# Kernel optimization log

Measured on AMD Instinct MI355X. Metric: run time of the kernel, lower is better.

## Reference

```python
import jax, jax.numpy as jnp
import numpy as np
from jax import lax

L, B, T, C, F = 4, 4, 2048, 1024, 4096  # n_layer, batch, ctx_len, n_embd(=dim_att), dim_ffn
EPS = 1e-5


def setup_inputs() -> dict:
    key = jax.random.key(0)
    ks = jax.random.split(key, 16)
    s = 0.02
    d = {}
    d["x"] = jax.random.normal(ks[0], (B, T, C), jnp.float32)
    d["ln0_w"] = jnp.ones((C,), jnp.float32)
    d["ln0_b"] = jnp.zeros((C,), jnp.float32)
    d["ln1_w"] = jnp.ones((L, C), jnp.float32)
    d["ln1_b"] = jnp.zeros((L, C), jnp.float32)
    d["ln2_w"] = jnp.ones((L, C), jnp.float32)
    d["ln2_b"] = jnp.zeros((L, C), jnp.float32)
    d["time_decay"] = jax.random.normal(ks[1], (L, C), jnp.float32) * 0.5
    d["time_first"] = jax.random.normal(ks[2], (L, C), jnp.float32) * 0.5 + jnp.float32(np.log(0.3))
    d["tmk"] = jax.random.uniform(ks[3], (L, C), jnp.float32)
    d["tmv"] = jax.random.uniform(ks[4], (L, C), jnp.float32)
    d["tmr"] = jax.random.uniform(ks[5], (L, C), jnp.float32)
    d["Wk"] = jax.random.normal(ks[6], (L, C, C), jnp.float32) * s
    d["Wv"] = jax.random.normal(ks[7], (L, C, C), jnp.float32) * s
    d["Wr"] = jax.random.normal(ks[8], (L, C, C), jnp.float32) * s
    d["Wo"] = jax.random.normal(ks[9], (L, C, C), jnp.float32) * s
    d["cmk"] = jax.random.uniform(ks[10], (L, C), jnp.float32)
    d["cmr"] = jax.random.uniform(ks[11], (L, C), jnp.float32)
    d["Wck"] = jax.random.normal(ks[12], (L, F, C), jnp.float32) * s  # key: n_embd -> dim_ffn
    d["Wcv"] = jax.random.normal(ks[13], (L, C, F), jnp.float32) * s  # value: dim_ffn -> n_embd
    d["Wcr"] = jax.random.normal(ks[14], (L, C, C), jnp.float32) * s  # receptance
    return d


def layernorm(x, w, b):
    m = jnp.mean(x, axis=-1, keepdims=True)
    v = jnp.var(x, axis=-1, keepdims=True)
    return (x - m) * lax.rsqrt(v + EPS) * w + b


def time_shift(x):
    # ZeroPad2d((0,0,1,-1)): shift sequence right by one, zero at t=0
    return jnp.pad(x, ((0, 0), (1, 0), (0, 0)))[:, :-1]


def wkv(time_decay, time_first, k, v):
    # numerically-stable RWKV-4 WKV recurrence; k,v: [B,T,C]
    w = -jnp.exp(time_decay)  # [C]
    u = time_first            # [C]
    kt = jnp.swapaxes(k, 0, 1)  # [T,B,C]
    vt = jnp.swapaxes(v, 0, 1)
    Bn, Cn = k.shape[0], k.shape[2]
    init = (jnp.zeros((Bn, Cn), k.dtype), jnp.zeros((Bn, Cn), k.dtype),
            jnp.full((Bn, Cn), -1e38, k.dtype))

    def step(carry, kv):
        aa, bb, pp = carry
        kk, vv = kv
        ww = u + kk
        qq = jnp.maximum(pp, ww)
        e1 = jnp.exp(pp - qq)
        e2 = jnp.exp(ww - qq)
        out = (e1 * aa + e2 * vv) / (e1 * bb + e2)
        ww2 = pp + w
        qq2 = jnp.maximum(ww2, kk)
        e1b = jnp.exp(ww2 - qq2)
        e2b = jnp.exp(kk - qq2)
        return (e1b * aa + e2b * vv, e1b * bb + e2b, qq2), out

    _, out = lax.scan(step, init, (kt, vt))
    return jnp.swapaxes(out, 0, 1)  # [B,T,C]


def reference(x, ln0_w, ln0_b, ln1_w, ln1_b, ln2_w, ln2_b, time_decay, time_first,
              tmk, tmv, tmr, Wk, Wv, Wr, Wo, cmk, cmr, Wck, Wcv, Wcr):
    x = layernorm(x, ln0_w, ln0_b)  # ln0 on layer 0
    for l in range(L):
        # --- TimeMix ---
        h = layernorm(x, ln1_w[l], ln1_b[l])
        hh = time_shift(h)
        xk = h * tmk[l] + hh * (1 - tmk[l])
        xv = h * tmv[l] + hh * (1 - tmv[l])
        xr = h * tmr[l] + hh * (1 - tmr[l])
        k = jnp.einsum('btc,oc->bto', xk, Wk[l])
        v = jnp.einsum('btc,oc->bto', xv, Wv[l])
        sr = jax.nn.sigmoid(jnp.einsum('btc,oc->bto', xr, Wr[l]))
        rwkv = sr * wkv(time_decay[l], time_first[l], k, v)
        x = x + jnp.einsum('bto,co->btc', rwkv, Wo[l])
        # --- ChannelMix ---
        h = layernorm(x, ln2_w[l], ln2_b[l])
        hh = time_shift(h)
        xk = h * cmk[l] + hh * (1 - cmk[l])
        xr = h * cmr[l] + hh * (1 - cmr[l])
        kf = jnp.einsum('btc,fc->btf', xk, Wck[l])
        kf = jnp.square(jax.nn.relu(kf))
        kv = jnp.einsum('btf,cf->btc', kf, Wcv[l])
        x = x + jax.nn.sigmoid(jnp.einsum('btc,oc->bto', xr, Wcr[l])) * kv
    return x
```

## Files before the change

kernel.cpp:

```cpp
#include <hip/hip_runtime.h>
#include <cstdint>

#define TT 2048
#define CCH 1024
#define FFD 4096
#define EPSV 1e-5f
#define NCHK 32
#define CHKL 64

typedef __attribute__((ext_vector_type(4))) float floatx4;
typedef __attribute__((ext_vector_type(8))) short shortx8;

__device__ __forceinline__ unsigned short f32_to_bf16(float f){
  union { float f; unsigned int u; } x; x.f = f;
  unsigned int r = x.u + 0x7fffu + ((x.u >> 16) & 1u);
  return (unsigned short)(r >> 16);
}
__device__ __forceinline__ float bf16_to_f32(unsigned short h){
  union { unsigned int u; float f; } x; x.u = ((unsigned int)h) << 16;
  return x.f;
}
__device__ __forceinline__ float wave_sum(float v){
  #pragma unroll
  for (int o = 32; o > 0; o >>= 1) v += __shfl_down(v, o, 64);
  return v;
}
__device__ __forceinline__ void async16(const void* g, void* l){
  __builtin_amdgcn_global_load_lds((const __attribute__((address_space(1))) void*)g,
                                   (__attribute__((address_space(3))) void*)l, 16, 0, 0);
}

struct CvtArgs {
  const float* s[7];
  unsigned short* d[7];
  int n4[7];
};
__global__ __launch_bounds__(256) void cvt7_kernel(CvtArgs a){
  const int seg = blockIdx.y;
  const float* __restrict__ s = a.s[seg];
  unsigned short* __restrict__ d = a.d[seg];
  const int n4 = a.n4[seg];
  for (int i = blockIdx.x * 256 + threadIdx.x; i < n4; i += gridDim.x * 256) {
    float4 v = ((const float4*)s)[i];
    union { unsigned short u[4]; uint2 p; } o;
    o.u[0] = f32_to_bf16(v.x); o.u[1] = f32_to_bf16(v.y);
    o.u[2] = f32_to_bf16(v.z); o.u[3] = f32_to_bf16(v.w);
    *(uint2*)&d[(long)i * 4] = o.p;
  }
}

__global__ __launch_bounds__(256) void ln0_kernel(const float* __restrict__ xin,
    const float* __restrict__ w, const float* __restrict__ b, float* __restrict__ xo){
  const int row = blockIdx.x, tid = threadIdx.x;
  const float* xr = xin + (long)row * CCH;
  float c4[4]; float s = 0.f, s2 = 0.f;
  #pragma unroll
  for (int j = 0; j < 4; j++){ c4[j] = xr[tid + j*256]; s += c4[j]; s2 += c4[j]*c4[j]; }
  s = wave_sum(s); s2 = wave_sum(s2);
  __shared__ float red[2][4];
  const int wid = tid >> 6, lane = tid & 63;
  if (lane == 0){ red[0][wid] = s; red[1][wid] = s2; }
  __syncthreads();
  const float S  = red[0][0]+red[0][1]+red[0][2]+red[0][3];
  const float S2 = red[1][0]+red[1][1]+red[1][2]+red[1][3];
  const float inv = 1.f / CCH;
  const float m = S * inv;
  const float rs = rsqrtf(S2 * inv - m*m + EPSV);
  float* xout = xo + (long)row * CCH;
  #pragma unroll
  for (int j = 0; j < 4; j++){ int c = tid + j*256; xout[c] = (c4[j]-m)*rs*w[c] + b[c]; }
}

template<int NOUT>
__global__ __launch_bounds__(256) void ln_mix(
    const float* __restrict__ x,
    const float* __restrict__ lw, const float* __restrict__ lb,
    const float* __restrict__ mk, const float* __restrict__ mv, const float* __restrict__ mr,
    unsigned short* __restrict__ xk, unsigned short* __restrict__ xv, unsigned short* __restrict__ xr)
{
  const int row = blockIdx.x;
  const int t = row & (TT - 1);
  const int tid = threadIdx.x;
  const float* xc = x + (long)row * CCH;
  const float* xp = xc - CCH;
  float c4[4], p4[4];
  float s1=0.f, s2=0.f, s3=0.f, s4=0.f;
  #pragma unroll
  for (int j = 0; j < 4; j++){
    const int c = tid + j*256;
    c4[j] = xc[c];
    p4[j] = (t > 0) ? xp[c] : 0.f;
    s1 += c4[j]; s2 += c4[j]*c4[j];
    s3 += p4[j]; s4 += p4[j]*p4[j];
  }
  s1 = wave_sum(s1); s2 = wave_sum(s2); s3 = wave_sum(s3); s4 = wave_sum(s4);
  __shared__ float red[4][4];
  const int wid = tid >> 6, lane = tid & 63;
  if (lane == 0){ red[wid][0]=s1; red[wid][1]=s2; red[wid][2]=s3; red[wid][3]=s4; }
  __syncthreads();
  const float S1 = red[0][0]+red[1][0]+red[2][0]+red[3][0];
  const float S2 = red[0][1]+red[1][1]+red[2][1]+red[3][1];
  const float S3 = red[0][2]+red[1][2]+red[2][2]+red[3][2];
  const float S4 = red[0][3]+red[1][3]+red[2][3]+red[3][3];
  const float inv = 1.f / CCH;
  const float m1 = S1*inv; const float r1 = rsqrtf(S2*inv - m1*m1 + EPSV);
  const float m0 = S3*inv; const float r0 = rsqrtf(S4*inv - m0*m0 + EPSV);
  #pragma unroll
  for (int j = 0; j < 4; j++){
    const int c = tid + j*256;
    const long o = (long)row * CCH + c;
    const float wv = lw[c], bv = lb[c];
    const float h  = (c4[j]-m1)*r1*wv + bv;
    const float hp = (t > 0) ? ((p4[j]-m0)*r0*wv + bv) : 0.f;
    const float a = mk[c]; xk[o] = f32_to_bf16(h*a + hp*(1.f-a));
    if (NOUT == 3){ const float q = mv[c]; xv[o] = f32_to_bf16(h*q + hp*(1.f-q)); }
    const float g = mr[c]; xr[o] = f32_to_bf16(h*g + hp*(1.f-g));
  }
}

__global__ __launch_bounds__(256) void wkv_pass1(
    const unsigned short* __restrict__ kin, const unsigned short* __restrict__ vin,
    const float* __restrict__ td,
    float* __restrict__ sta, float* __restrict__ stb, float* __restrict__ stp)
{
  const int c = blockIdx.x * 256 + threadIdx.x;
  const int chunk = blockIdx.y, b = blockIdx.z;
  const float w = -__expf(td[c]);
  const long base = ((long)b * TT + (long)chunk * CHKL) * CCH + c;
  float aa = 0.f, bb = 0.f, pp = -1e38f;
  for (int t0 = 0; t0 < CHKL; t0 += 8) {
    float kr[8], vr[8];
    #pragma unroll
    for (int j = 0; j < 8; j++){
      const long o = base + (long)(t0 + j) * CCH;
      kr[j] = bf16_to_f32(kin[o]);
      vr[j] = bf16_to_f32(vin[o]);
    }
    #pragma unroll
    for (int j = 0; j < 8; j++){
      const float kk = kr[j], vv = vr[j];
      const float ww2 = pp + w;
      const float qq2 = fmaxf(ww2, kk);
      const float e1b = __expf(ww2 - qq2), e2b = __expf(kk - qq2);
      aa = e1b*aa + e2b*vv; bb = e1b*bb + e2b; pp = qq2;
    }
  }
  const long si = (long)chunk * 4096 + b * CCH + c;
  sta[si] = aa; stb[si] = bb; stp[si] = pp;
}

__global__ __launch_bounds__(256) void wkv_combine(
    const float* __restrict__ td,
    const float* __restrict__ sta, const float* __restrict__ stb, const float* __restrict__ stp,
    float* __restrict__ ina, float* __restrict__ inb, float* __restrict__ inp)
{
  const int idx = blockIdx.x * 256 + threadIdx.x;
  const int c = idx & (CCH - 1);
  const float wn = -__expf(td[c]) * (float)CHKL;
  float a = 0.f, b = 0.f, p = -1e38f;
  for (int j0 = 0; j0 < NCHK; j0 += 8) {
    float la[8], lb[8], lp[8];
    #pragma unroll
    for (int j = 0; j < 8; j++){
      const long si = (long)(j0 + j) * 4096 + idx;
      la[j] = sta[si]; lb[j] = stb[si]; lp[j] = stp[si];
    }
    #pragma unroll
    for (int j = 0; j < 8; j++){
      const long si = (long)(j0 + j) * 4096 + idx;
      ina[si] = a; inb[si] = b; inp[si] = p;
      const float pd = p + wn;
      const float q = fmaxf(pd, lp[j]);
      const float e1 = __expf(pd - q), e2 = __expf(lp[j] - q);
      a = e1*a + e2*la[j]; b = e1*b + e2*lb[j]; p = q;
    }
  }
}

__global__ __launch_bounds__(256) void wkv_pass2(
    const unsigned short* __restrict__ kin, const unsigned short* __restrict__ vin,
    const unsigned short* __restrict__ srin,
    const float* __restrict__ td, const float* __restrict__ tf,
    const float* __restrict__ ina, const float* __restrict__ inb, const float* __restrict__ inp,
    unsigned short* __restrict__ out)
{
  const int c = blockIdx.x * 256 + threadIdx.x;
  const int chunk = blockIdx.y, b = blockIdx.z;
  const float w = -__expf(td[c]);
  const float u = tf[c];
  const long si = (long)chunk * 4096 + b * CCH + c;
  float aa = ina[si], bb = inb[si], pp = inp[si];
  const long base = ((long)b * TT + (long)chunk * CHKL) * CCH + c;
  for (int t0 = 0; t0 < CHKL; t0 += 8) {
    float kr[8], vr[8], sr[8];
    #pragma unroll
    for (int j = 0; j < 8; j++){
      const long o = base + (long)(t0 + j) * CCH;
      kr[j] = bf16_to_f32(kin[o]);
      vr[j] = bf16_to_f32(vin[o]);
      sr[j] = bf16_to_f32(srin[o]);
    }
    #pragma unroll
    for (int j = 0; j < 8; j++){
      const float kk = kr[j], vv = vr[j];
      const float ww = u + kk;
      const float qq = fmaxf(pp, ww);
      const float e1 = __expf(pp - qq), e2 = __expf(ww - qq);
      const float outv = (e1*aa + e2*vv) / (e1*bb + e2);
      const float ww2 = pp + w;
      const float qq2 = fmaxf(ww2, kk);
      const float e1b = __expf(ww2 - qq2), e2b = __expf(kk - qq2);
      aa = e1b*aa + e2b*vv; bb = e1b*bb + e2b; pp = qq2;
      out[base + (long)(t0 + j) * CCH] = f32_to_bf16(sr[j] * outv);
    }
  }
}

#define BM 128
#define BN 128
#define BK 64

enum { EP_BF16 = 0, EP_ADD = 3, EP_MULADD = 4, EP_KVR = 5, EP_FFN1 = 6 };

template<int EPI>
__global__ __launch_bounds__(256) void gemm_bt(
    const unsigned short* __restrict__ A,
    const unsigned short* __restrict__ W,
    int N, const int K,
    unsigned short* __restrict__ outb,
    float* __restrict__ xres,
    const unsigned short* __restrict__ rr,
    const unsigned short* __restrict__ A2,
    const unsigned short* __restrict__ W2,
    unsigned short* __restrict__ outb2,
    const int N2)
{
  const int bm = blockIdx.x;
  int bn = blockIdx.y;
  bool sig = false;
  if (EPI == EP_KVR) {
    const long z = blockIdx.z;
    const long Mfull = (long)gridDim.x * BM;
    A    += z * Mfull * K;
    W    += z * (long)N * K;
    outb += z * Mfull * N;
    sig = (blockIdx.z == 2);
  }
  if (EPI == EP_FFN1) {
    if (blockIdx.z == 1) {
      if (bn >= N2 / BN) return;
      A = A2; W = W2; outb = outb2; N = N2; sig = true;
    }
  }
  __shared__ unsigned short lA[BM * BK];
  __shared__ unsigned short lW[BN * BK];
  const int tid = threadIdx.x;
  const int wid = tid >> 6, lane = tid & 63;
  const int wm = (wid >> 1) * 64, wn = (wid & 1) * 64;
  const int quad = lane >> 4, r16 = lane & 15;

  const int srow = tid >> 3;
  const int scol = (tid & 7) ^ (srow & 7);
  const unsigned short* Ag = A + ((long)(bm * BM + srow)) * K + scol * 8;
  const unsigned short* Wg = W + ((long)(bn * BN + srow)) * K + scol * 8;
  const long rs32 = (long)32 * K;

  const int sw0 = ((quad)     ^ (r16 & 7)) * 8;
  const int sw1 = ((4 + quad) ^ (r16 & 7)) * 8;

  const floatx4 zf = {0.f, 0.f, 0.f, 0.f};
  floatx4 acc[4][4];
  #pragma unroll
  for (int i = 0; i < 4; i++)
    #pragma unroll
    for (int j = 0; j < 4; j++) acc[i][j] = zf;

  for (int k0 = 0; k0 < K; k0 += BK) {
    __syncthreads();
    #pragma unroll
    for (int i = 0; i < 4; i++) {
      async16(Ag + (long)i * rs32 + k0, &lA[(i * 256 + wid * 64) * 8]);
      async16(Wg + (long)i * rs32 + k0, &lW[(i * 256 + wid * 64) * 8]);
    }
    __syncthreads();
    #pragma unroll
    for (int kk = 0; kk < 2; kk++) {
      const int sw = kk ? sw1 : sw0;
      shortx8 af[4], bf[4];
      #pragma unroll
      for (int m = 0; m < 4; m++) af[m] = *(const shortx8*)&lA[(wm + m*16 + r16) * 64 + sw];
      #pragma unroll
      for (int n = 0; n < 4; n++) bf[n] = *(const shortx8*)&lW[(wn + n*16 + r16) * 64 + sw];
      #pragma unroll
      for (int m = 0; m < 4; m++)
        #pragma unroll
        for (int n = 0; n < 4; n++)
          acc[m][n] = __builtin_amdgcn_mfma_f32_16x16x32_bf16(af[m], bf[n], acc[m][n], 0, 0, 0);
    }
  }

  const int colBase = bn * BN + wn + r16;
  #pragma unroll
  for (int m = 0; m < 4; m++) {
    const int rowBase = bm * BM + wm + m * 16 + quad * 4;
    #pragma unroll
    for (int n = 0; n < 4; n++) {
      const int col = colBase + n * 16;
      #pragma unroll
      for (int r = 0; r < 4; r++) {
        const long idx = (long)(rowBase + r) * N + col;
        const float val = acc[m][n][r];
        if (EPI == EP_KVR)       outb[idx] = sig ? f32_to_bf16(1.f / (1.f + __expf(-val)))
                                                 : f32_to_bf16(val);
        else if (EPI == EP_FFN1) {
          if (sig) outb[idx] = f32_to_bf16(1.f / (1.f + __expf(-val)));
          else     { const float t = val > 0.f ? val : 0.f; outb[idx] = f32_to_bf16(t * t); }
        }
        else if (EPI == EP_ADD)  xres[idx] += val;
        else if (EPI == EP_MULADD) xres[idx] = fmaf(bf16_to_f32(rr[idx]), val, xres[idx]);
        else                     outb[idx] = f32_to_bf16(val);
      }
    }
  }
}

extern "C" void kernel_launch(void* const* d_in, const int* in_sizes, int n_in,
                              void* d_out, int out_size, void* d_ws, size_t ws_size,
                              hipStream_t stream)
{
  const float* x_in       = (const float*)d_in[0];
  const float* ln0_w      = (const float*)d_in[1];
  const float* ln0_b      = (const float*)d_in[2];
  const float* ln1_w      = (const float*)d_in[3];
  const float* ln1_b      = (const float*)d_in[4];
  const float* ln2_w      = (const float*)d_in[5];
  const float* ln2_b      = (const float*)d_in[6];
  const float* time_decay = (const float*)d_in[7];
  const float* time_first = (const float*)d_in[8];
  const float* tmk        = (const float*)d_in[9];
  const float* tmv        = (const float*)d_in[10];
  const float* tmr        = (const float*)d_in[11];
  const float* Wk         = (const float*)d_in[12];
  const float* Wv         = (const float*)d_in[13];
  const float* Wr         = (const float*)d_in[14];
  const float* Wo         = (const float*)d_in[15];
  const float* cmk        = (const float*)d_in[16];
  const float* cmr        = (const float*)d_in[17];
  const float* Wck        = (const float*)d_in[18];
  const float* Wcv        = (const float*)d_in[19];
  const float* Wcr        = (const float*)d_in[20];
  float* x = (float*)d_out;

  const int M = 4 * TT;
  const long lCC = (long)CCH * CCH;
  const long lFC = (long)FFD * CCH;
  const long MC  = (long)M * CCH;

  unsigned short* wsl  = (unsigned short*)d_ws;
  unsigned short* wkb  = wsl;
  unsigned short* wvb  = wkb + lCC;
  unsigned short* wrb  = wvb + lCC;
  unsigned short* wob  = wrb + lCC;
  unsigned short* wcrb = wob + lCC;
  unsigned short* wckb = wcrb + lCC;
  unsigned short* wcvb = wckb + lFC;
  unsigned short* xk   = wcvb + lFC;
  unsigned short* xv   = xk + MC;
  unsigned short* xr   = xv + MC;
  unsigned short* kbuf = xr + MC;
  unsigned short* vbuf = kbuf + MC;
  unsigned short* sbuf = vbuf + MC;
  unsigned short* kfb  = kbuf;
  unsigned short* rrb  = kbuf + (long)M * FFD;

  float* sta = (float*)xk;
  float* stb = sta + (long)NCHK * 4096;
  float* stp = stb + (long)NCHK * 4096;
  float* ina = stp + (long)NCHK * 4096;
  float* inb = ina + (long)NCHK * 4096;
  float* inp = inb + (long)NCHK * 4096;

  ln0_kernel<<<M, 256, 0, stream>>>(x_in, ln0_w, ln0_b, x);

  const dim3 g1(M / BM, CCH / BN);
  const dim3 gkvr(M / BM, CCH / BN, 3);
  const dim3 gffn(M / BM, FFD / BN, 2);
  const dim3 gw(CCH / 256, NCHK, 4);

  for (int l = 0; l < 4; l++) {
    CvtArgs ca;
    ca.s[0] = Wk  + (long)l * lCC; ca.d[0] = wkb;  ca.n4[0] = (int)(lCC / 4);
    ca.s[1] = Wv  + (long)l * lCC; ca.d[1] = wvb;  ca.n4[1] = (int)(lCC / 4);
    ca.s[2] = Wr  + (long)l * lCC; ca.d[2] = wrb;  ca.n4[2] = (int)(lCC / 4);
    ca.s[3] = Wo  + (long)l * lCC; ca.d[3] = wob;  ca.n4[3] = (int)(lCC / 4);
    ca.s[4] = Wcr + (long)l * lCC; ca.d[4] = wcrb; ca.n4[4] = (int)(lCC / 4);
    ca.s[5] = Wck + (long)l * lFC; ca.d[5] = wckb; ca.n4[5] = (int)(lFC / 4);
    ca.s[6] = Wcv + (long)l * lFC; ca.d[6] = wcvb; ca.n4[6] = (int)(lFC / 4);
    cvt7_kernel<<<dim3(512, 7), 256, 0, stream>>>(ca);

    const float* td_l = time_decay + l*CCH;
    const float* tf_l = time_first + l*CCH;

    ln_mix<3><<<M, 256, 0, stream>>>(x, ln1_w + l*CCH, ln1_b + l*CCH,
                                     tmk + l*CCH, tmv + l*CCH, tmr + l*CCH, xk, xv, xr);
    gemm_bt<EP_KVR><<<gkvr, 256, 0, stream>>>(xk, wkb, CCH, CCH, kbuf, nullptr, nullptr,
                                              nullptr, nullptr, nullptr, 0);
    wkv_pass1 <<<gw, 256, 0, stream>>>(kbuf, vbuf, td_l, sta, stb, stp);
    wkv_combine<<<16, 256, 0, stream>>>(td_l, sta, stb, stp, ina, inb, inp);
    wkv_pass2 <<<gw, 256, 0, stream>>>(kbuf, vbuf, sbuf, td_l, tf_l, ina, inb, inp, xv);
    gemm_bt<EP_ADD ><<<g1, 256, 0, stream>>>(xv, wob, CCH, CCH, nullptr, x, nullptr,
                                             nullptr, nullptr, nullptr, 0);

    ln_mix<2><<<M, 256, 0, stream>>>(x, ln2_w + l*CCH, ln2_b + l*CCH,
                                     cmk + l*CCH, nullptr, cmr + l*CCH, xk, nullptr, xr);
    gemm_bt<EP_FFN1><<<gffn, 256, 0, stream>>>(xk, wckb, FFD, CCH, kfb, nullptr, nullptr,
                                               xr, wcrb, rrb, CCH);
    gemm_bt<EP_MULADD><<<g1, 256, 0, stream>>>(kfb, wcvb, CCH, FFD, nullptr, x, rrb,
                                               nullptr, nullptr, nullptr, 0);
  }
}
```

Baseline: 1.800 ms.

## Rewrite GEMM with larger tiles, 512 threads and a four-slot async LDS pipeline

Replaces the single-buffered 128x128x64 GEMM with a templated kernel using 256-row tiles, 512-thread blocks and a four-slot shared-memory ring with K-step 32. Global loads are issued three stages ahead, with explicit vmcnt waits and a single barrier per step. MFMA sections run at raised priority. The aim is to overlap global-memory latency with matrix math and to reuse more data per tile. The cost is more registers, less occupancy per CU, and fewer blocks on the smaller GEMMs, where the grid shrinks to 32x8.

```diff
diff --git a/kernel.cpp b/kernel.cpp
--- a/kernel.cpp
+++ b/kernel.cpp
@@ -216,14 +216,14 @@
   }
 }
 
-#define BM 128
-#define BN 128
-#define BK 64
+#define BM 256
+#define BKQ 32
+#define NSLOT 4
 
 enum { EP_BF16 = 0, EP_ADD = 3, EP_MULADD = 4, EP_KVR = 5, EP_FFN1 = 6 };
 
-template<int EPI>
-__global__ __launch_bounds__(256) void gemm_bt(
+template<int EPI, int BNt, int WMv, int WNv>
+__global__ __launch_bounds__(512, 2) void gemm_bt(
     const unsigned short* __restrict__ A,
     const unsigned short* __restrict__ W,
     int N, const int K,
@@ -235,6 +235,12 @@
     unsigned short* __restrict__ outb2,
     const int N2)
 {
+  constexpr int MR  = BM  / WMv / 16;
+  constexpr int NR  = BNt / WNv / 16;
+  constexpr int LA  = (BM  * BKQ) / (512 * 8);
+  constexpr int LB  = (BNt * BKQ) / (512 * 8);
+  constexpr int LPT = LA + LB;
+
   const int bm = blockIdx.x;
   int bn = blockIdx.y;
   bool sig = false;
@@ -248,63 +254,101 @@
   }
   if (EPI == EP_FFN1) {
     if (blockIdx.z == 1) {
-      if (bn >= N2 / BN) return;
+      if (bn >= N2 / BNt) return;
       A = A2; W = W2; outb = outb2; N = N2; sig = true;
     }
   }
-  __shared__ unsigned short lA[BM * BK];
-  __shared__ unsigned short lW[BN * BK];
+
+  __shared__ unsigned short lA[NSLOT][BM  * BKQ];
+  __shared__ unsigned short lB[NSLOT][BNt * BKQ];
+
   const int tid = threadIdx.x;
   const int wid = tid >> 6, lane = tid & 63;
-  const int wm = (wid >> 1) * 64, wn = (wid & 1) * 64;
   const int quad = lane >> 4, r16 = lane & 15;
-
-  const int srow = tid >> 3;
-  const int scol = (tid & 7) ^ (srow & 7);
-  const unsigned short* Ag = A + ((long)(bm * BM + srow)) * K + scol * 8;
-  const unsigned short* Wg = W + ((long)(bn * BN + srow)) * K + scol * 8;
-  const long rs32 = (long)32 * K;
-
-  const int sw0 = ((quad)     ^ (r16 & 7)) * 8;
-  const int sw1 = ((4 + quad) ^ (r16 & 7)) * 8;
+  const int wm = wid / WNv, wn = wid % WNv;
+  const int WR = wm * (MR * 16);
+  const int WC = wn * (NR * 16);
+  const int swc = (quad ^ ((r16 >> 1) & 3)) * 8;
+
+  const unsigned short* aSrc[LA];
+  int aDst[LA];
+  #pragma unroll
+  for (int i = 0; i < LA; i++) {
+    const int P = i * 512 + tid;
+    const int row = P >> 2;
+    const int c = (P & 3) ^ ((row >> 1) & 3);
+    aSrc[i] = A + (long)(bm * BM + row) * K + c * 8;
+    aDst[i] = P * 8;
+  }
+  const unsigned short* bSrc[LB];
+  int bDst[LB];
+  #pragma unroll
+  for (int i = 0; i < LB; i++) {
+    const int P = i * 512 + tid;
+    const int row = P >> 2;
+    const int c = (P & 3) ^ ((row >> 1) & 3);
+    bSrc[i] = W + (long)(bn * BNt + row) * K + c * 8;
+    bDst[i] = P * 8;
+  }
 
   const floatx4 zf = {0.f, 0.f, 0.f, 0.f};
-  floatx4 acc[4][4];
-  #pragma unroll
-  for (int i = 0; i < 4; i++)
-    #pragma unroll
-    for (int j = 0; j < 4; j++) acc[i][j] = zf;
-
-  for (int k0 = 0; k0 < K; k0 += BK) {
-    __syncthreads();
-    #pragma unroll
-    for (int i = 0; i < 4; i++) {
-      async16(Ag + (long)i * rs32 + k0, &lA[(i * 256 + wid * 64) * 8]);
-      async16(Wg + (long)i * rs32 + k0, &lW[(i * 256 + wid * 64) * 8]);
-    }
-    __syncthreads();
-    #pragma unroll
-    for (int kk = 0; kk < 2; kk++) {
-      const int sw = kk ? sw1 : sw0;
-      shortx8 af[4], bf[4];
+  floatx4 acc[MR][NR];
+  #pragma unroll
+  for (int i = 0; i < MR; i++)
+    #pragma unroll
+    for (int j = 0; j < NR; j++) acc[i][j] = zf;
+
+  const int NT = K / BKQ;
+
+  auto stage = [&](int tt){
+    const int sl = tt & (NSLOT - 1);
+    const long ko = (long)tt * BKQ;
+    #pragma unroll
+    for (int i = 0; i < LA; i++) async16(aSrc[i] + ko, &lA[sl][aDst[i]]);
+    #pragma unroll
+    for (int i = 0; i < LB; i++) async16(bSrc[i] + ko, &lB[sl][bDst[i]]);
+  };
+
+  stage(0); stage(1); stage(2);
+  asm volatile("s_waitcnt vmcnt(%0)" :: "n"(2 * LPT) : "memory");
+  __builtin_amdgcn_s_barrier();
+  __builtin_amdgcn_sched_barrier(0);
+
+  for (int t = 0; t < NT; ++t) {
+    if (t + 3 < NT) stage(t + 3);
+    const int s = t & (NSLOT - 1);
+    shortx8 af[MR];
+    #pragma unroll
+    for (int m = 0; m < MR; m++)
+      af[m] = *(const shortx8*)&lA[s][(WR + m * 16 + r16) * BKQ + swc];
+    #pragma unroll
+    for (int nh = 0; nh < NR; nh += 2) {
+      const shortx8 b0 = *(const shortx8*)&lB[s][(WC + (nh    ) * 16 + r16) * BKQ + swc];
+      const shortx8 b1 = *(const shortx8*)&lB[s][(WC + (nh + 1) * 16 + r16) * BKQ + swc];
+      __builtin_amdgcn_s_setprio(1);
       #pragma unroll
-      for (int m = 0; m < 4; m++) af[m] = *(const shortx8*)&lA[(wm + m*16 + r16) * 64 + sw];
+      for (int m = 0; m < MR; m++)
+        acc[m][nh    ] = __builtin_amdgcn_mfma_f32_16x16x32_bf16(af[m], b0, acc[m][nh    ], 0, 0, 0);
       #pragma unroll
-      for (int n = 0; n < 4; n++) bf[n] = *(const shortx8*)&lW[(wn + n*16 + r16) * 64 + sw];
-      #pragma unroll
-      for (int m = 0; m < 4; m++)
-        #pragma unroll
-        for (int n = 0; n < 4; n++)
-          acc[m][n] = __builtin_amdgcn_mfma_f32_16x16x32_bf16(af[m], bf[n], acc[m][n], 0, 0, 0);
-    }
-  }
-
-  const int colBase = bn * BN + wn + r16;
-  #pragma unroll
-  for (int m = 0; m < 4; m++) {
-    const int rowBase = bm * BM + wm + m * 16 + quad * 4;
-    #pragma unroll
-    for (int n = 0; n < 4; n++) {
+      for (int m = 0; m < MR; m++)
+        acc[m][nh + 1] = __builtin_amdgcn_mfma_f32_16x16x32_bf16(af[m], b1, acc[m][nh + 1], 0, 0, 0);
+      __builtin_amdgcn_s_setprio(0);
+    }
+    if (t < NT - 3)       asm volatile("s_waitcnt vmcnt(%0)" :: "n"(2 * LPT) : "memory");
+    else if (t == NT - 3) asm volatile("s_waitcnt vmcnt(%0)" :: "n"(LPT) : "memory");
+    else if (t == NT - 2) asm volatile("s_waitcnt vmcnt(0)" ::: "memory");
+    if (t < NT - 1) {
+      __builtin_amdgcn_s_barrier();
+      __builtin_amdgcn_sched_barrier(0);
+    }
+  }
+
+  const int colBase = bn * BNt + WC + r16;
+  #pragma unroll
+  for (int m = 0; m < MR; m++) {
+    const int rowBase = bm * BM + WR + m * 16 + quad * 4;
+    #pragma unroll
+    for (int n = 0; n < NR; n++) {
       const int col = colBase + n * 16;
       #pragma unroll
       for (int r = 0; r < 4; r++) {
@@ -382,9 +426,9 @@
 
   ln0_kernel<<<M, 256, 0, stream>>>(x_in, ln0_w, ln0_b, x);
 
-  const dim3 g1(M / BM, CCH / BN);
-  const dim3 gkvr(M / BM, CCH / BN, 3);
-  const dim3 gffn(M / BM, FFD / BN, 2);
+  const dim3 gkvr(M / BM, CCH / 256, 3);
+  const dim3 g1n (M / BM, CCH / 128);
+  const dim3 gffn(M / BM, FFD / 256, 2);
   const dim3 gw(CCH / 256, NCHK, 4);
 
   for (int l = 0; l < 4; l++) {
@@ -403,19 +447,19 @@
 
     ln_mix<3><<<M, 256, 0, stream>>>(x, ln1_w + l*CCH, ln1_b + l*CCH,
                                      tmk + l*CCH, tmv + l*CCH, tmr + l*CCH, xk, xv, xr);
-    gemm_bt<EP_KVR><<<gkvr, 256, 0, stream>>>(xk, wkb, CCH, CCH, kbuf, nullptr, nullptr,
-                                              nullptr, nullptr, nullptr, 0);
+    gemm_bt<EP_KVR, 256, 2, 4><<<gkvr, 512, 0, stream>>>(xk, wkb, CCH, CCH, kbuf, nullptr,
+                                              nullptr, nullptr, nullptr, nullptr, 0);
     wkv_pass1 <<<gw, 256, 0, stream>>>(kbuf, vbuf, td_l, sta, stb, stp);
     wkv_combine<<<16, 256, 0, stream>>>(td_l, sta, stb, stp, ina, inb, inp);
     wkv_pass2 <<<gw, 256, 0, stream>>>(kbuf, vbuf, sbuf, td_l, tf_l, ina, inb, inp, xv);
-    gemm_bt<EP_ADD ><<<g1, 256, 0, stream>>>(xv, wob, CCH, CCH, nullptr, x, nullptr,
-                                             nullptr, nullptr, nullptr, 0);
+    gemm_bt<EP_ADD, 128, 4, 2><<<g1n, 512, 0, stream>>>(xv, wob, CCH, CCH, nullptr, x,
+                                             nullptr, nullptr, nullptr, nullptr, 0);
 
     ln_mix<2><<<M, 256, 0, stream>>>(x, ln2_w + l*CCH, ln2_b + l*CCH,
                                      cmk + l*CCH, nullptr, cmr + l*CCH, xk, nullptr, xr);
-    gemm_bt<EP_FFN1><<<gffn, 256, 0, stream>>>(xk, wckb, FFD, CCH, kfb, nullptr, nullptr,
-                                               xr, wcrb, rrb, CCH);
-    gemm_bt<EP_MULADD><<<g1, 256, 0, stream>>>(kfb, wcvb, CCH, FFD, nullptr, x, rrb,
-                                               nullptr, nullptr, nullptr, 0);
-  }
-}
+    gemm_bt<EP_FFN1, 256, 2, 4><<<gffn, 512, 0, stream>>>(xk, wckb, FFD, CCH, kfb, nullptr,
+                                               nullptr, xr, wcrb, rrb, CCH);
+    gemm_bt<EP_MULADD, 128, 4, 2><<<g1n, 512, 0, stream>>>(kfb, wcvb, CCH, FFD, nullptr, x,
+                                               rrb, nullptr, nullptr, nullptr, 0);
+  }
+}
```

New measurement: 2.067 ms. 14.9% more time.
